# Kernel tuning notes

Measured on AMD Instinct MI355X. Metric: run time of the kernel, lower is better.

Reference implementation:

```python
import jax, jax.numpy as jnp
import numpy as np

N = 262144      # total atoms (ragged over batch)
B = 64          # batch_size
K = 16          # retrieved features per sample
H = 256         # h_dim
R = 512         # ret_feat_dim


def setup_inputs() -> dict:
    key = jax.random.key(0)
    k1, k2, k3, k4, k5, k6, k7 = jax.random.split(key, 7)
    h = jax.random.normal(k1, (N, H), dtype=jnp.float32)
    ret_feat = jax.random.normal(k2, (B, K, R), dtype=jnp.float32)
    batch = jnp.sort(jax.random.randint(k3, (N,), 0, B, dtype=jnp.int64))
    # nn.Linear weights: y = x @ W.T + b
    Wp = jax.random.normal(k4, (H, R), dtype=jnp.float32) / np.sqrt(R)
    bp = jax.random.normal(k5, (H,), dtype=jnp.float32) * 0.01
    Wl = jax.random.normal(k6, (H, 2 * H), dtype=jnp.float32) / np.sqrt(2 * H)
    bl = jax.random.normal(k7, (H,), dtype=jnp.float32) * 0.01
    return {"h": h, "ret_feat": ret_feat, "batch": batch,
            "Wp": Wp, "bp": bp, "Wl": Wl, "bl": bl}


def reference(h, ret_feat, batch, Wp, bp, Wl, bl):
    # ret_feat: [B, K, R] -> mean over K -> project to [B, H]
    ret = jnp.mean(ret_feat, axis=1)                    # [B, R]
    ret = ret @ Wp.T + bp                               # [B, H]
    # The torch loop gathers h[batch==i], concats the pooled feature
    # repeated per atom, applies `linear`, and scatters back. Since every
    # atom is covered exactly once, this is a per-node gather + linear:
    per_node = ret[batch]                               # [N, H] gather
    x = jnp.concatenate([h, per_node], axis=-1)         # [N, 2H]
    return x @ Wl.T + bl                                # [N, H]
```

## Files before the change

### kernel.cpp

```cpp
#include <hip/hip_runtime.h>
#include <hip/hip_bf16.h>

#define N_ATOMS 262144
#define B_SZ    64
#define H_DIM   256
#define R_DIM   512

#define TILE_ROWS 64
#define NBLOCKS   (N_ATOMS / TILE_ROWS)

typedef __attribute__((ext_vector_type(8))) short bf16x8;
typedef __attribute__((ext_vector_type(4))) float f32x4;

static __device__ __forceinline__ short f2bf(float f) {
  unsigned u = __builtin_bit_cast(unsigned, f);
  u = (u + 0x7FFFu + ((u >> 16) & 1u)) >> 16;
  return (short)u;
}

static __device__ __forceinline__ unsigned cvtpk(float lo, float hi) {
  unsigned r;
  asm("v_cvt_pk_bf16_f32 %0, %1, %2" : "=v"(r) : "v"(lo), "v"(hi));
  return r;
}

static __device__ __forceinline__ bf16x8 pack8(f32x4 a0, f32x4 a1) {
  unsigned u0 = cvtpk(a0[0], a0[1]);
  unsigned u1 = cvtpk(a0[2], a0[3]);
  unsigned u2 = cvtpk(a1[0], a1[1]);
  unsigned u3 = cvtpk(a1[2], a1[3]);
  bf16x8 v;
  v[0] = (short)(u0 & 0xFFFF); v[1] = (short)(u0 >> 16);
  v[2] = (short)(u1 & 0xFFFF); v[3] = (short)(u1 >> 16);
  v[4] = (short)(u2 & 0xFFFF); v[5] = (short)(u2 >> 16);
  v[6] = (short)(u3 & 0xFFFF); v[7] = (short)(u3 >> 16);
  return v;
}

__global__ __launch_bounds__(1024) void prep_kernel(
    const float* __restrict__ rf, const float* __restrict__ Wp,
    const float* __restrict__ bp, const float* __restrict__ Wl,
    const float* __restrict__ bl, float* __restrict__ pooled,
    short* __restrict__ Bbf) {
  int t = threadIdx.x;
  if (blockIdx.x >= B_SZ) {
    int base = (blockIdx.x - B_SZ) * 4096 + t * 4;
#pragma unroll
    for (int q = 0; q < 4; ++q) {
      int idx  = base + q;
      int j    = idx & 7;
      int lane = (idx >> 3) & 63;
      int ks   = (idx >> 9) & 7;
      int ct   = idx >> 12;
      int o    = ct * 16 + (lane & 15);
      int k    = ks * 32 + ((lane >> 4) << 3) + j;
      Bbf[idx] = f2bf(Wl[o * (2 * H_DIM) + k]);
    }
    return;
  }

  __shared__ float meanr[R_DIM];
  __shared__ float retj[H_DIM];
  int b    = blockIdx.x;
  int lane = t & 63;
  int w    = t >> 6;

  if (t < R_DIM) {
    float s = 0.f;
    const float* p = rf + (long)b * 16 * R_DIM + t;
#pragma unroll
    for (int k = 0; k < 16; ++k) s += p[k * R_DIM];
    meanr[t] = s * (1.f / 16.f);
  }
  __syncthreads();

  {
    f32x4 m0 = *(const f32x4*)&meanr[lane * 8];
    f32x4 m1 = *(const f32x4*)&meanr[lane * 8 + 4];
#pragma unroll
    for (int jj = 0; jj < 16; ++jj) {
      int j = w * 16 + jj;
      const f32x4* wp = (const f32x4*)(Wp + (long)j * R_DIM + lane * 8);
      f32x4 w0 = wp[0], w1 = wp[1];
      float s = m0[0]*w0[0] + m0[1]*w0[1] + m0[2]*w0[2] + m0[3]*w0[3]
              + m1[0]*w1[0] + m1[1]*w1[1] + m1[2]*w1[2] + m1[3]*w1[3];
#pragma unroll
      for (int d = 1; d < 64; d <<= 1) s += __shfl_xor(s, d);
      if (lane == 0) retj[j] = s + bp[j];
    }
  }
  __syncthreads();

  {
    f32x4 r0 = *(const f32x4*)&retj[lane * 4];
#pragma unroll
    for (int oo = 0; oo < 16; ++oo) {
      int o = w * 16 + oo;
      f32x4 wv = *(const f32x4*)(Wl + (long)o * (2 * H_DIM) + H_DIM + lane * 4);
      float s = r0[0]*wv[0] + r0[1]*wv[1] + r0[2]*wv[2] + r0[3]*wv[3];
#pragma unroll
      for (int d = 1; d < 64; d <<= 1) s += __shfl_xor(s, d);
      if (lane == 0) pooled[b * H_DIM + o] = s + bl[o];
    }
  }
}

__global__ __launch_bounds__(512, 4) void gemm_kernel(
    const float* __restrict__ h, const short* __restrict__ Bbf,
    const float* __restrict__ pooled, const int* __restrict__ batch,
    float* __restrict__ out) {
  __shared__ short As[32 * 64 * 8];
  int t    = threadIdx.x;
  int lane = t & 63;
  int w    = t >> 6;
  const int arow = lane & 15;
  const int kg   = lane >> 4;
  long m0 = (long)blockIdx.x * TILE_ROWS;

  bf16x8 bfrag0[8], bfrag1[8];
#pragma unroll
  for (int ks = 0; ks < 8; ++ks) {
    bfrag0[ks] = *(const bf16x8*)(Bbf + ((((2 * w)     * 8 + ks) * 64 + lane) << 3));
    bfrag1[ks] = *(const bf16x8*)(Bbf + ((((2 * w + 1) * 8 + ks) * 64 + lane) << 3));
  }

#pragma unroll
  for (int i = 0; i < 4; ++i) {
    int S   = 4 * w + i;
    int row = ((S >> 3) << 4) + arow;
    int kf  = ((S & 7) << 5) + (kg << 3);
    const float* p = h + (m0 + row) * H_DIM + kf;
    f32x4 a0 = *(const f32x4*)p;
    f32x4 a1 = *(const f32x4*)(p + 4);
    *(bf16x8*)&As[(S * 64 + lane) << 3] = pack8(a0, a1);
  }
  __syncthreads();

  int o0 = ((2 * w) << 4) + (kg << 2);
  int o1 = o0 + 16;
#pragma unroll
  for (int rt = 0; rt < 4; ++rt) {
    f32x4 acc0 = {0.f, 0.f, 0.f, 0.f};
    f32x4 acc1 = {0.f, 0.f, 0.f, 0.f};
#pragma unroll
    for (int ks = 0; ks < 8; ++ks) {
      bf16x8 af = *(const bf16x8*)&As[((rt * 8 + ks) * 64 + lane) << 3];
      acc0 = __builtin_amdgcn_mfma_f32_16x16x32_bf16(bfrag0[ks], af, acc0, 0, 0, 0);
      acc1 = __builtin_amdgcn_mfma_f32_16x16x32_bf16(bfrag1[ks], af, acc1, 0, 0, 0);
    }
    long row = m0 + rt * 16 + arow;
    int  b   = batch[row];
    const float* pb = pooled + b * H_DIM;
    f32x4 pv0 = *(const f32x4*)(pb + o0);
    f32x4 pv1 = *(const f32x4*)(pb + o1);
    float* orow = out + row * H_DIM;
    *(f32x4*)(orow + o0) = acc0 + pv0;
    *(f32x4*)(orow + o1) = acc1 + pv1;
  }
}

extern "C" void kernel_launch(void* const* d_in, const int* in_sizes, int n_in,
                              void* d_out, int out_size, void* d_ws, size_t ws_size,
                              hipStream_t stream) {
  const float* h   = (const float*)d_in[0];
  const float* rf  = (const float*)d_in[1];
  const int*   bat = (const int*)d_in[2];
  const float* Wp  = (const float*)d_in[3];
  const float* bp  = (const float*)d_in[4];
  const float* Wl  = (const float*)d_in[5];
  const float* bl  = (const float*)d_in[6];
  float* out = (float*)d_out;

  float* pooled = (float*)d_ws;
  short* Bbf    = (short*)((char*)d_ws + 64 * 1024);

  prep_kernel<<<B_SZ + 16, 1024, 0, stream>>>(rf, Wp, bp, Wl, bl, pooled, Bbf);
  gemm_kernel<<<NBLOCKS, 512, 0, stream>>>(h, Bbf, pooled, bat, out);
}
```

Measured before the change: 158.6 us.

## Make GEMM persistent with double-buffered async global-to-LDS loads of h

Each GEMM block now handles 16 tiles of 32 rows instead of one 64-row tile. It double-buffers fp32 h tiles in LDS using global_load_lds async copies, so the load of the next tile overlaps MFMA work on the current one. The fp32-to-bf16 conversion moves from the staging step to just before each MFMA, and the B fragments are loaded once per block instead of once per 64 rows. The price is fewer blocks (512), twice the LDS, and extra conversion work in the inner loop. The sync after the async copies may not wait for global_load_lds to finish without an explicit vmcnt wait, so correctness is a risk.

```diff
diff --git a/kernel.cpp b/kernel.cpp
--- a/kernel.cpp
+++ b/kernel.cpp
@@ -6,8 +6,9 @@
 #define H_DIM   256
 #define R_DIM   512
 
-#define TILE_ROWS 64
-#define NBLOCKS   (N_ATOMS / TILE_ROWS)
+#define TILE_ROWS 32
+#define TPB       16
+#define NBLOCKS   (N_ATOMS / (TILE_ROWS * TPB))
 
 typedef __attribute__((ext_vector_type(8))) short bf16x8;
 typedef __attribute__((ext_vector_type(4))) float f32x4;
@@ -37,6 +38,13 @@
   return v;
 }
 
+static __device__ __forceinline__ void async_copy16(const float* g, short* lds) {
+  __builtin_amdgcn_global_load_lds(
+      (const __attribute__((address_space(1))) unsigned int*)g,
+      (__attribute__((address_space(3))) unsigned int*)lds,
+      16, 0, 0);
+}
+
 __global__ __launch_bounds__(1024) void prep_kernel(
     const float* __restrict__ rf, const float* __restrict__ Wp,
     const float* __restrict__ bp, const float* __restrict__ Wl,
@@ -109,13 +117,12 @@
     const float* __restrict__ h, const short* __restrict__ Bbf,
     const float* __restrict__ pooled, const int* __restrict__ batch,
     float* __restrict__ out) {
-  __shared__ short As[32 * 64 * 8];
+  __shared__ short As[2][32 * 512];
   int t    = threadIdx.x;
   int lane = t & 63;
   int w    = t >> 6;
   const int arow = lane & 15;
   const int kg   = lane >> 4;
-  long m0 = (long)blockIdx.x * TILE_ROWS;
 
   bf16x8 bfrag0[8], bfrag1[8];
 #pragma unroll
@@ -124,38 +131,62 @@
     bfrag1[ks] = *(const bf16x8*)(Bbf + ((((2 * w + 1) * 8 + ks) * 64 + lane) << 3));
   }
 
+  int S_[4], row_[4], col_[4];
 #pragma unroll
   for (int i = 0; i < 4; ++i) {
     int S   = 4 * w + i;
-    int row = ((S >> 3) << 4) + arow;
-    int kf  = ((S & 7) << 5) + (kg << 3);
-    const float* p = h + (m0 + row) * H_DIM + kf;
-    f32x4 a0 = *(const f32x4*)p;
-    f32x4 a1 = *(const f32x4*)(p + 4);
-    *(bf16x8*)&As[(S * 64 + lane) << 3] = pack8(a0, a1);
-  }
+    S_[i]   = S;
+    row_[i] = ((S >> 4) << 4) + arow;
+    col_[i] = (((S >> 1) & 7) << 5) + (kg << 3) + ((S & 1) << 2);
+  }
+
+  long base_row = (long)blockIdx.x * (TILE_ROWS * TPB);
+
+#pragma unroll
+  for (int i = 0; i < 4; ++i)
+    async_copy16(h + (base_row + row_[i]) * H_DIM + col_[i],
+                 &As[0][S_[i] * 512]);
   __syncthreads();
 
   int o0 = ((2 * w) << 4) + (kg << 2);
   int o1 = o0 + 16;
-#pragma unroll
-  for (int rt = 0; rt < 4; ++rt) {
-    f32x4 acc0 = {0.f, 0.f, 0.f, 0.f};
-    f32x4 acc1 = {0.f, 0.f, 0.f, 0.f};
-#pragma unroll
-    for (int ks = 0; ks < 8; ++ks) {
-      bf16x8 af = *(const bf16x8*)&As[((rt * 8 + ks) * 64 + lane) << 3];
-      acc0 = __builtin_amdgcn_mfma_f32_16x16x32_bf16(bfrag0[ks], af, acc0, 0, 0, 0);
-      acc1 = __builtin_amdgcn_mfma_f32_16x16x32_bf16(bfrag1[ks], af, acc1, 0, 0, 0);
-    }
-    long row = m0 + rt * 16 + arow;
-    int  b   = batch[row];
-    const float* pb = pooled + b * H_DIM;
-    f32x4 pv0 = *(const f32x4*)(pb + o0);
-    f32x4 pv1 = *(const f32x4*)(pb + o1);
-    float* orow = out + row * H_DIM;
-    *(f32x4*)(orow + o0) = acc0 + pv0;
-    *(f32x4*)(orow + o1) = acc1 + pv1;
+
+  for (int tt = 0; tt < TPB; ++tt) {
+    int  buf = tt & 1;
+    long g0  = base_row + (long)tt * TILE_ROWS;
+
+    if (tt + 1 < TPB) {
+      long gn = g0 + TILE_ROWS;
+#pragma unroll
+      for (int i = 0; i < 4; ++i)
+        async_copy16(h + (gn + row_[i]) * H_DIM + col_[i],
+                     &As[buf ^ 1][S_[i] * 512]);
+    }
+
+#pragma unroll
+    for (int rt = 0; rt < 2; ++rt) {
+      f32x4 acc0 = {0.f, 0.f, 0.f, 0.f};
+      f32x4 acc1 = {0.f, 0.f, 0.f, 0.f};
+#pragma unroll
+      for (int ks = 0; ks < 8; ++ks) {
+        int S0 = rt * 16 + ks * 2;
+        f32x4 v0 = *(const f32x4*)&As[buf][(S0 * 512) + lane * 8];
+        f32x4 v1 = *(const f32x4*)&As[buf][((S0 + 1) * 512) + lane * 8];
+        bf16x8 af = pack8(v0, v1);
+        acc0 = __builtin_amdgcn_mfma_f32_16x16x32_bf16(bfrag0[ks], af, acc0, 0, 0, 0);
+        acc1 = __builtin_amdgcn_mfma_f32_16x16x32_bf16(bfrag1[ks], af, acc1, 0, 0, 0);
+      }
+      long row = g0 + rt * 16 + arow;
+      int  b   = batch[row];
+      const float* pb = pooled + b * H_DIM;
+      f32x4 pv0 = *(const f32x4*)(pb + o0);
+      f32x4 pv1 = *(const f32x4*)(pb + o1);
+      float* orow = out + row * H_DIM;
+      *(f32x4*)(orow + o0) = acc0 + pv0;
+      *(f32x4*)(orow + o1) = acc1 + pv1;
+    }
+
+    __syncthreads();
   }
 }
 
```

New measurement: 149.3 us. -5.8%, faster.

## Make GEMM persistent over 512 rows with register-prefetched A and LDS pooled cache

Applied to the files above, without the earlier changes.

Each block now handles 512 rows instead of 64, so the per-block load of the full bf16 weight fragments is amortised over many more rows. The A tile is no longer staged through LDS. Instead, each wave loads the h rows straight into registers, converts them to bf16 in place, and prefetches the next 16-row set while the current MFMAs run. Pooled rows for the block's batch range are cached in LDS when the span is at most 16 samples, and batch offsets are precomputed once per block. The trade-offs are fewer blocks (512) with higher register use and duplicated loads of h across waves, which can reduce latency hiding.

```diff
diff --git a/kernel.cpp b/kernel.cpp
--- a/kernel.cpp
+++ b/kernel.cpp
@@ -6,8 +6,9 @@
 #define H_DIM   256
 #define R_DIM   512
 
-#define TILE_ROWS 64
-#define NBLOCKS   (N_ATOMS / TILE_ROWS)
+#define ROWS_PB 512
+#define NSETS   32
+#define NBLOCKS (N_ATOMS / ROWS_PB)
 
 typedef __attribute__((ext_vector_type(8))) short bf16x8;
 typedef __attribute__((ext_vector_type(4))) float f32x4;
@@ -105,17 +106,18 @@
   }
 }
 
-__global__ __launch_bounds__(512, 4) void gemm_kernel(
+__global__ __launch_bounds__(512) void gemm_kernel(
     const float* __restrict__ h, const short* __restrict__ Bbf,
     const float* __restrict__ pooled, const int* __restrict__ batch,
     float* __restrict__ out) {
-  __shared__ short As[32 * 64 * 8];
+  __shared__ float pooled_lds[16 * 256];
+  __shared__ short boff_lds[512];
   int t    = threadIdx.x;
   int lane = t & 63;
   int w    = t >> 6;
   const int arow = lane & 15;
   const int kg   = lane >> 4;
-  long m0 = (long)blockIdx.x * TILE_ROWS;
+  long base_row = (long)blockIdx.x * ROWS_PB;
 
   bf16x8 bfrag0[8], bfrag1[8];
 #pragma unroll
@@ -124,36 +126,68 @@
     bfrag1[ks] = *(const bf16x8*)(Bbf + ((((2 * w + 1) * 8 + ks) * 64 + lane) << 3));
   }
 
-#pragma unroll
-  for (int i = 0; i < 4; ++i) {
-    int S   = 4 * w + i;
-    int row = ((S >> 3) << 4) + arow;
-    int kf  = ((S & 7) << 5) + (kg << 3);
-    const float* p = h + (m0 + row) * H_DIM + kf;
-    f32x4 a0 = *(const f32x4*)p;
-    f32x4 a1 = *(const f32x4*)(p + 4);
-    *(bf16x8*)&As[(S * 64 + lane) << 3] = pack8(a0, a1);
-  }
+  int b_t     = batch[base_row + t];
+  int b_first = batch[base_row];
+  int b_last  = batch[base_row + ROWS_PB - 1];
+  int span    = b_last - b_first + 1;
+  boff_lds[t] = (short)(b_t - b_first);
+  const bool small_span = (span <= 16);
+  if (small_span) {
+    int fi = t * 8;
+    if (fi < span * H_DIM) {
+      *(f32x4*)&pooled_lds[fi]     = *(const f32x4*)(pooled + (long)b_first * H_DIM + fi);
+      *(f32x4*)&pooled_lds[fi + 4] = *(const f32x4*)(pooled + (long)b_first * H_DIM + fi + 4);
+    }
+  }
+
+  const float* ap0 = h + (base_row + arow) * H_DIM + (kg << 3);
+  f32x4 av[8][2];
+#pragma unroll
+  for (int ks = 0; ks < 8; ++ks) {
+    av[ks][0] = *(const f32x4*)(ap0 + ks * 32);
+    av[ks][1] = *(const f32x4*)(ap0 + ks * 32 + 4);
+  }
+
   __syncthreads();
 
-  int o0 = ((2 * w) << 4) + (kg << 2);
+  int o0 = (w << 5) + (kg << 2);
   int o1 = o0 + 16;
-#pragma unroll
-  for (int rt = 0; rt < 4; ++rt) {
+
+  for (int s = 0; s < NSETS; ++s) {
+    long g0 = base_row + (long)s * 16;
+    int  sn = (s + 1 < NSETS) ? s + 1 : s;
+    const float* apn = h + (base_row + (long)sn * 16 + arow) * H_DIM + (kg << 3);
+
     f32x4 acc0 = {0.f, 0.f, 0.f, 0.f};
     f32x4 acc1 = {0.f, 0.f, 0.f, 0.f};
-#pragma unroll
-    for (int ks = 0; ks < 8; ++ks) {
-      bf16x8 af = *(const bf16x8*)&As[((rt * 8 + ks) * 64 + lane) << 3];
-      acc0 = __builtin_amdgcn_mfma_f32_16x16x32_bf16(bfrag0[ks], af, acc0, 0, 0, 0);
-      acc1 = __builtin_amdgcn_mfma_f32_16x16x32_bf16(bfrag1[ks], af, acc1, 0, 0, 0);
-    }
-    long row = m0 + rt * 16 + arow;
-    int  b   = batch[row];
-    const float* pb = pooled + b * H_DIM;
-    f32x4 pv0 = *(const f32x4*)(pb + o0);
-    f32x4 pv1 = *(const f32x4*)(pb + o1);
-    float* orow = out + row * H_DIM;
+
+#pragma unroll
+    for (int b = 0; b < 4; ++b) {
+      int k0 = 2 * b, k1 = 2 * b + 1;
+      bf16x8 af0 = pack8(av[k0][0], av[k0][1]);
+      bf16x8 af1 = pack8(av[k1][0], av[k1][1]);
+      av[k0][0] = *(const f32x4*)(apn + k0 * 32);
+      av[k0][1] = *(const f32x4*)(apn + k0 * 32 + 4);
+      av[k1][0] = *(const f32x4*)(apn + k1 * 32);
+      av[k1][1] = *(const f32x4*)(apn + k1 * 32 + 4);
+      __builtin_amdgcn_sched_barrier(0);
+      acc0 = __builtin_amdgcn_mfma_f32_16x16x32_bf16(bfrag0[k0], af0, acc0, 0, 0, 0);
+      acc1 = __builtin_amdgcn_mfma_f32_16x16x32_bf16(bfrag1[k0], af0, acc1, 0, 0, 0);
+      acc0 = __builtin_amdgcn_mfma_f32_16x16x32_bf16(bfrag0[k1], af1, acc0, 0, 0, 0);
+      acc1 = __builtin_amdgcn_mfma_f32_16x16x32_bf16(bfrag1[k1], af1, acc1, 0, 0, 0);
+    }
+
+    int off = (int)boff_lds[s * 16 + arow];
+    f32x4 pv0, pv1;
+    if (small_span) {
+      pv0 = *(const f32x4*)&pooled_lds[(off << 8) + o0];
+      pv1 = *(const f32x4*)&pooled_lds[(off << 8) + o1];
+    } else {
+      const float* pb = pooled + (long)(b_first + off) * H_DIM;
+      pv0 = *(const f32x4*)(pb + o0);
+      pv1 = *(const f32x4*)(pb + o1);
+    }
+    float* orow = out + (g0 + arow) * H_DIM;
     *(f32x4*)(orow + o0) = acc0 + pv0;
     *(f32x4*)(orow + o1) = acc1 + pv1;
   }
```

Result: slower. 294.3 us (+85.6%).
